# Performance work log

Hardware: AMD Instinct MI355X
Metric: run time of the kernel (lower is better)

The kernel has to match this reference:

```python
import jax, jax.numpy as jnp
import numpy as np

TRIM = 0.2
BIG = jnp.float32(1e30)  # sentinel pushing invalid pixels to the sorted tail


def setup_inputs() -> dict:
    key = jax.random.key(0)
    k1, k2, k3 = jax.random.split(key, 3)
    B, H, W = 32, 480, 640
    prediction = jax.random.normal(k1, (B, H, W), dtype=jnp.float32)
    target = jax.random.normal(k2, (B, H, W), dtype=jnp.float32)
    mask = jax.random.randint(k3, (B, H, W), 0, 2).astype(jnp.int32)
    return {"prediction": prediction, "target": target, "mask": mask}


def reference(prediction, target, mask):
    maskb = mask.astype(bool)
    M_total = jnp.sum(maskb)  # total number of valid pixels (== M.sum() in torch)
    abs_res = jnp.abs(prediction - target)
    # invalid pixels -> BIG so they sort to the end and are trimmed away
    flat = jnp.where(maskb, abs_res, BIG).reshape(-1)
    sorted_res = jnp.sort(flat)
    # keep the smallest int(num_valid * (1 - trim)) residuals
    k = jnp.floor(M_total.astype(jnp.float32) * (1.0 - TRIM)).astype(jnp.int32)
    keep = jnp.arange(flat.shape[0]) < k
    batch_loss = jnp.sum(jnp.where(keep, sorted_res, jnp.float32(0.0)))
    denom = 2.0 * M_total.astype(jnp.float32)
    # guard against fully-invalid mask (torch returns 0.0 in that case)
    return jnp.where(M_total > 0, batch_loss / jnp.maximum(denom, 1.0), jnp.float32(0.0))
```

## Files before the change

kernel.cpp:

```cpp
#include <hip/hip_runtime.h>

#define THREADS 256
#define NWAVE 4
#define NBLK 1920
#define NBINS 256
#define RPER 16
#define RBLK (NBLK / RPER)
#define QSCALE 32768.0f
#define MASK40 ((1ull << 40) - 1ull)
#define UNROLL 5


__global__ __launch_bounds__(THREADS) void k_hist(
    const float* __restrict__ pred, const float* __restrict__ targ,
    const int* __restrict__ mask, unsigned long long* __restrict__ hist_part,
    unsigned long long* __restrict__ fcnt, unsigned long long* __restrict__ fq,
    int N)
{
  __shared__ unsigned long long lh[NWAVE][NBINS];
  for (int i = threadIdx.x; i < NWAVE * NBINS; i += THREADS)
    ((unsigned long long*)lh)[i] = 0ull;
  if (blockIdx.x == 0) {
    for (int i = threadIdx.x; i < NBINS; i += THREADS) { fcnt[i] = 0ull; fq[i] = 0ull; }
  }
  __syncthreads();

  const int wave = threadIdx.x >> 6;
  const int gtid = blockIdx.x * THREADS + threadIdx.x;
  const int gsz  = gridDim.x * THREADS;
  const int n4   = N >> 2;
  const int steps = n4 / gsz;
  const int rem   = n4 - steps * gsz;

  auto acc = [&](float pv, float tv, int valid) {
    if (valid) {
      const float r = fabsf(pv - tv);
      const unsigned int b = (unsigned int)fminf(r * 32.0f, 255.0f);
      const unsigned long long q =
          (unsigned long long)(unsigned int)(fminf(r, 8.0f) * QSCALE + 0.5f);
      atomicAdd(&lh[wave][b], (1ull << 40) | q);
    }
  };

  const float4* p4 = (const float4*)pred;
  const float4* t4 = (const float4*)targ;
  const int4*   m4 = (const int4*)mask;

  int s = 0;
  for (; s + UNROLL <= steps; s += UNROLL) {
    float4 P[UNROLL], T[UNROLL];
    int4   Mv[UNROLL];
#pragma unroll
    for (int u = 0; u < UNROLL; ++u) {
      const int i = gtid + (s + u) * gsz;
      P[u] = p4[i]; T[u] = t4[i]; Mv[u] = m4[i];
    }
#pragma unroll
    for (int u = 0; u < UNROLL; ++u) {
      acc(P[u].x, T[u].x, Mv[u].x); acc(P[u].y, T[u].y, Mv[u].y);
      acc(P[u].z, T[u].z, Mv[u].z); acc(P[u].w, T[u].w, Mv[u].w);
    }
  }
  for (; s < steps; ++s) {
    const int i = gtid + s * gsz;
    const float4 p = p4[i]; const float4 t = t4[i]; const int4 m = m4[i];
    acc(p.x, t.x, m.x); acc(p.y, t.y, m.y); acc(p.z, t.z, m.z); acc(p.w, t.w, m.w);
  }
  if (rem && gtid < rem) {
    const int i = gtid + steps * gsz;
    const float4 p = p4[i]; const float4 t = t4[i]; const int4 m = m4[i];
    acc(p.x, t.x, m.x); acc(p.y, t.y, m.y); acc(p.z, t.z, m.z); acc(p.w, t.w, m.w);
  }
  for (int i = (n4 << 2) + gtid; i < N; i += gsz)
    acc(pred[i], targ[i], mask[i]);

  __syncthreads();
  const int t = threadIdx.x;
  const unsigned long long v = lh[0][t] + lh[1][t] + lh[2][t] + lh[3][t];
  hist_part[(size_t)blockIdx.x * NBINS + t] = v;
}

__global__ __launch_bounds__(THREADS) void k_reduce(
    const unsigned long long* __restrict__ hist_part,
    unsigned long long* __restrict__ fcnt, unsigned long long* __restrict__ fq)
{
  const int t = threadIdx.x;
  unsigned long long c = 0ull, q = 0ull;
  const int base = blockIdx.x * RPER;
  for (int p = base; p < base + RPER; ++p) {
    const unsigned long long v = hist_part[(size_t)p * NBINS + t];
    c += v >> 40;
    q += v & MASK40;
  }
  if (c) atomicAdd(&fcnt[t], c);
  if (q) atomicAdd(&fq[t], q);
}

__global__ __launch_bounds__(THREADS) void k_final(
    const unsigned long long* __restrict__ fcnt,
    const unsigned long long* __restrict__ fq, float* __restrict__ out)
{
  __shared__ unsigned long long sc[NBINS];
  __shared__ unsigned long long sq[NBINS];
  const int t = threadIdx.x;
  sc[t] = fcnt[t];
  sq[t] = fq[t];
  __syncthreads();
  if (t == 0) {
    unsigned long long M64 = 0ull;
    for (int b = 0; b < NBINS; ++b) M64 += sc[b];
    float res = 0.f;
    if (M64 > 0ull) {
      const unsigned int M = (unsigned int)M64;
      const unsigned int k = (unsigned int)floorf((float)M * 0.8f);
      if (k > 0u) {
        unsigned long long cum = 0ull, qbelow = 0ull;
        int tb = NBINS - 1;
        for (int b = 0; b < NBINS; ++b) {
          const unsigned long long c = sc[b];
          if (cum + c >= (unsigned long long)k) { tb = b; break; }
          cum += c;
          qbelow += sq[b];
        }
        double sum_below = (double)qbelow / (double)QSCALE;
        const unsigned long long cnt_tb = sc[tb];
        if ((unsigned long long)k > cum && cnt_tb > 0ull) {
          const double mean_tb = ((double)sq[tb] / (double)QSCALE) / (double)cnt_tb;
          sum_below += (double)(k - (unsigned int)cum) * mean_tb;
        }
        double denom = 2.0 * (double)M;
        if (denom < 1.0) denom = 1.0;
        res = (float)(sum_below / denom);
      }
    }
    out[0] = res;
  }
}

extern "C" void kernel_launch(void* const* d_in, const int* in_sizes, int n_in,
                              void* d_out, int out_size, void* d_ws, size_t ws_size,
                              hipStream_t stream)
{
  const float* pred = (const float*)d_in[0];
  const float* targ = (const float*)d_in[1];
  const int*   mask = (const int*)d_in[2];
  float* out = (float*)d_out;
  const int N = in_sizes[0];

  char* ws = (char*)d_ws;
  unsigned long long* fcnt      = (unsigned long long*)ws;
  unsigned long long* fq        = (unsigned long long*)(ws + 2048);
  unsigned long long* hist_part = (unsigned long long*)(ws + 8192);

  k_hist  <<<NBLK, THREADS, 0, stream>>>(pred, targ, mask, hist_part, fcnt, fq, N);
  k_reduce<<<RBLK, THREADS, 0, stream>>>(hist_part, fcnt, fq);
  k_final <<<1,    THREADS, 0, stream>>>(fcnt, fq, out);
}
```

Measured before the change: 37.07 us.

## Double-buffer histogram loads, halve grid, and split LDS histogram per half-wave

Replaces the batch-of-five unrolled load loop with a two-deep software pipeline that issues the next tile's loads before consuming the current one. The grid is halved to 960 blocks so each thread handles more iterations. The LDS histogram is split into 8 copies, one per 32-thread half-wave, which cuts atomic contention at the cost of more shared memory and a longer final merge. Fewer loads are in flight per thread than with the five-deep unroll, which may expose more memory latency.

After: 34.75 us, median of 2. 6.3% less time.

```diff
diff --git a/kernel.cpp b/kernel.cpp
--- a/kernel.cpp
+++ b/kernel.cpp
@@ -1,14 +1,13 @@
 #include <hip/hip_runtime.h>
 
 #define THREADS 256
-#define NWAVE 4
-#define NBLK 1920
+#define NSUB 8
+#define NBLK 960
 #define NBINS 256
 #define RPER 16
 #define RBLK (NBLK / RPER)
 #define QSCALE 32768.0f
 #define MASK40 ((1ull << 40) - 1ull)
-#define UNROLL 5
 
 
 __global__ __launch_bounds__(THREADS) void k_hist(
@@ -17,20 +16,18 @@
     unsigned long long* __restrict__ fcnt, unsigned long long* __restrict__ fq,
     int N)
 {
-  __shared__ unsigned long long lh[NWAVE][NBINS];
-  for (int i = threadIdx.x; i < NWAVE * NBINS; i += THREADS)
+  __shared__ unsigned long long lh[NSUB][NBINS];
+  for (int i = threadIdx.x; i < NSUB * NBINS; i += THREADS)
     ((unsigned long long*)lh)[i] = 0ull;
   if (blockIdx.x == 0) {
     for (int i = threadIdx.x; i < NBINS; i += THREADS) { fcnt[i] = 0ull; fq[i] = 0ull; }
   }
   __syncthreads();
 
-  const int wave = threadIdx.x >> 6;
+  const int sub  = threadIdx.x >> 5;
   const int gtid = blockIdx.x * THREADS + threadIdx.x;
   const int gsz  = gridDim.x * THREADS;
   const int n4   = N >> 2;
-  const int steps = n4 / gsz;
-  const int rem   = n4 - steps * gsz;
 
   auto acc = [&](float pv, float tv, int valid) {
     if (valid) {
@@ -38,7 +35,7 @@
       const unsigned int b = (unsigned int)fminf(r * 32.0f, 255.0f);
       const unsigned long long q =
           (unsigned long long)(unsigned int)(fminf(r, 8.0f) * QSCALE + 0.5f);
-      atomicAdd(&lh[wave][b], (1ull << 40) | q);
+      atomicAdd(&lh[sub][b], (1ull << 40) | q);
     }
   };
 
@@ -46,37 +43,45 @@
   const float4* t4 = (const float4*)targ;
   const int4*   m4 = (const int4*)mask;
 
-  int s = 0;
-  for (; s + UNROLL <= steps; s += UNROLL) {
-    float4 P[UNROLL], T[UNROLL];
-    int4   Mv[UNROLL];
-#pragma unroll
-    for (int u = 0; u < UNROLL; ++u) {
-      const int i = gtid + (s + u) * gsz;
-      P[u] = p4[i]; T[u] = t4[i]; Mv[u] = m4[i];
+#define CONSUME(P, T, M)                                        \
+  do {                                                          \
+    acc((P).x, (T).x, (M).x); acc((P).y, (T).y, (M).y);         \
+    acc((P).z, (T).z, (M).z); acc((P).w, (T).w, (M).w);         \
+  } while (0)
+
+  const int steps = n4 / gsz;
+  if (steps * gsz == n4 && steps >= 2) {
+    float4 pA = p4[gtid],       tA = t4[gtid];       int4 mA = m4[gtid];
+    float4 pB = p4[gtid + gsz], tB = t4[gtid + gsz]; int4 mB = m4[gtid + gsz];
+    int s = 0;
+    for (; s + 3 < steps; s += 2) {
+      CONSUME(pA, tA, mA);
+      { const int i = gtid + (s + 2) * gsz; pA = p4[i]; tA = t4[i]; mA = m4[i]; }
+      CONSUME(pB, tB, mB);
+      { const int i = gtid + (s + 3) * gsz; pB = p4[i]; tB = t4[i]; mB = m4[i]; }
     }
-#pragma unroll
-    for (int u = 0; u < UNROLL; ++u) {
-      acc(P[u].x, T[u].x, Mv[u].x); acc(P[u].y, T[u].y, Mv[u].y);
-      acc(P[u].z, T[u].z, Mv[u].z); acc(P[u].w, T[u].w, Mv[u].w);
+    CONSUME(pA, tA, mA);
+    CONSUME(pB, tB, mB);
+    for (int r = s + 2; r < steps; ++r) {
+      const int i = gtid + r * gsz;
+      const float4 p = p4[i]; const float4 t = t4[i]; const int4 m = m4[i];
+      CONSUME(p, t, m);
     }
-  }
-  for (; s < steps; ++s) {
-    const int i = gtid + s * gsz;
-    const float4 p = p4[i]; const float4 t = t4[i]; const int4 m = m4[i];
-    acc(p.x, t.x, m.x); acc(p.y, t.y, m.y); acc(p.z, t.z, m.z); acc(p.w, t.w, m.w);
-  }
-  if (rem && gtid < rem) {
-    const int i = gtid + steps * gsz;
-    const float4 p = p4[i]; const float4 t = t4[i]; const int4 m = m4[i];
-    acc(p.x, t.x, m.x); acc(p.y, t.y, m.y); acc(p.z, t.z, m.z); acc(p.w, t.w, m.w);
+  } else {
+    for (int i = gtid; i < n4; i += gsz) {
+      const float4 p = p4[i]; const float4 t = t4[i]; const int4 m = m4[i];
+      CONSUME(p, t, m);
+    }
   }
   for (int i = (n4 << 2) + gtid; i < N; i += gsz)
     acc(pred[i], targ[i], mask[i]);
+#undef CONSUME
 
   __syncthreads();
   const int t = threadIdx.x;
-  const unsigned long long v = lh[0][t] + lh[1][t] + lh[2][t] + lh[3][t];
+  unsigned long long v = 0ull;
+#pragma unroll
+  for (int c = 0; c < NSUB; ++c) v += lh[c][t];
   hist_part[(size_t)blockIdx.x * NBINS + t] = v;
 }
 
```
